# Kernel tuning notes

Hardware: AMD Instinct MI355X
Metric: run time of the kernel (lower is better)

## Reference

```python
import jax, jax.numpy as jnp
import numpy as np

N_NODES = 100000
N_EDGES = 3200000
N_IN = 128
N_HID = 128
N_OUT = 64
HOP = 10


def setup_inputs() -> dict:
    key = jax.random.key(0)
    ks = jax.random.split(key, 8)
    x = jax.random.normal(ks[0], (N_NODES, N_IN), dtype=jnp.float32)
    edge_row = jax.random.randint(ks[1], (N_EDGES,), 0, N_NODES, dtype=jnp.int32)
    edge_col = jax.random.randint(ks[2], (N_EDGES,), 0, N_NODES, dtype=jnp.int32)
    # normalized-ish edge weights so 10 hops of propagation stay bounded
    edge_val = jax.random.uniform(ks[3], (N_EDGES,), dtype=jnp.float32) / 32.0
    s_ih = 1.0 / np.sqrt(N_IN)
    s_hh = 1.0 / np.sqrt(N_HID)
    W_ih = jax.random.normal(ks[4], (4 * N_HID, N_IN), dtype=jnp.float32) * s_ih
    W_hh = jax.random.normal(ks[5], (4 * N_HID, N_HID), dtype=jnp.float32) * s_hh
    b_ih = jnp.zeros((4 * N_HID,), dtype=jnp.float32)
    b_hh = jnp.zeros((4 * N_HID,), dtype=jnp.float32)
    fc_w = jax.random.normal(ks[6], (N_OUT, N_HID), dtype=jnp.float32) * s_hh
    fc_b = jnp.zeros((N_OUT,), dtype=jnp.float32)
    return dict(x=x, edge_row=edge_row, edge_col=edge_col, edge_val=edge_val,
                W_ih=W_ih, W_hh=W_hh, b_ih=b_ih, b_hh=b_hh, fc_w=fc_w, fc_b=fc_b)


def _lstm_cell(x, h, c, W_ih, W_hh, b_ih, b_hh):
    # torch LSTMCell gate order: input, forget, cell(g), output
    gates = x @ W_ih.T + b_ih + h @ W_hh.T + b_hh  # [N, 4H]
    i, f, g, o = jnp.split(gates, 4, axis=-1)
    i = jax.nn.sigmoid(i)
    f = jax.nn.sigmoid(f)
    g = jnp.tanh(g)
    o = jax.nn.sigmoid(o)
    c_new = f * c + i * g
    h_new = o * jnp.tanh(c_new)
    return h_new, c_new


def _spmm(edge_row, edge_col, edge_val, h, n_nodes):
    # (A @ h)[r] = sum_{edges e with row r} val[e] * h[col[e]]
    msgs = edge_val[:, None] * h[edge_col]  # [E, H] gather
    return jax.ops.segment_sum(msgs, edge_row, num_segments=n_nodes)


def reference(x, edge_row, edge_col, edge_val, W_ih, W_hh, b_ih, b_hh, fc_w, fc_b):
    n = x.shape[0]
    h = jnp.zeros((n, W_hh.shape[1]), dtype=x.dtype)
    c = jnp.zeros_like(h)
    # hop iterations: LSTM gate update then sparse propagation (dropout = eval/identity)
    for _ in range(HOP):
        h, c = _lstm_cell(x, h, c, W_ih, W_hh, b_ih, b_hh)
        h = _spmm(edge_row, edge_col, edge_val, h, n)
    h = jax.nn.relu(h)
    return h @ fc_w.T + fc_b
```

## Files before the change

kernel.cpp:

```cpp
#include <hip/hip_runtime.h>
#include <hip/hip_bf16.h>
#include <math.h>

constexpr int NN  = 100000;
constexpr int EE  = 3200000;
constexpr int HID = 128;
constexpr int NG  = 512;
constexpr int NOUT = 64;
constexpr int HOPS = 10;
constexpr int SCAN_BLK = 1024;
constexpr int NBLK_SCAN = (NN + SCAN_BLK - 1) / SCAN_BLK;

typedef __attribute__((ext_vector_type(8))) short short8;
typedef __attribute__((ext_vector_type(4))) float f32x4;

__device__ __forceinline__ ushort f2bf(float f) {
    uint u = __builtin_bit_cast(uint, f);
    u += 0x7fff + ((u >> 16) & 1);
    return (ushort)(u >> 16);
}
__device__ __forceinline__ float bflo(uint u) { return __builtin_bit_cast(float, u << 16); }
__device__ __forceinline__ float bfhi(uint u) { return __builtin_bit_cast(float, u & 0xffff0000u); }

__device__ __forceinline__ float sigf(float v) { return 1.0f / (1.0f + __expf(-v)); }
__device__ __forceinline__ float tanh_fast(float x) {
    float t = __expf(-2.0f * fabsf(x));
    float r = (1.0f - t) / (1.0f + t);
    return copysignf(r, x);
}

__device__ __forceinline__ short8 load_frag(const ushort* p) {
    return *reinterpret_cast<const short8*>(p);
}
__device__ __forceinline__ f32x4 mfma16(short8 a, short8 b, f32x4 c) {
    return __builtin_amdgcn_mfma_f32_16x16x32_bf16(a, b, c, 0, 0, 0);
}

__global__ __launch_bounds__(256) void convert_bf16_kernel(
    const float* __restrict__ src, ushort* __restrict__ dst, int n4)
{
    int i = blockIdx.x * 256 + threadIdx.x;
    if (i < n4) {
        float4 v = reinterpret_cast<const float4*>(src)[i];
        ushort4 o;
        o.x = f2bf(v.x); o.y = f2bf(v.y); o.z = f2bf(v.z); o.w = f2bf(v.w);
        reinterpret_cast<ushort4*>(dst)[i] = o;
    }
}

__global__ __launch_bounds__(256) void bsum_kernel(
    const float* __restrict__ bih, const float* __restrict__ bhh, float* __restrict__ bsum)
{
    int i = blockIdx.x * 256 + threadIdx.x;
    if (i < NG) bsum[i] = bih[i] + bhh[i];
}

__global__ __launch_bounds__(256) void hist_kernel(const int* __restrict__ erow,
                                                   int* __restrict__ deg)
{
    int e = blockIdx.x * 256 + threadIdx.x;
    atomicAdd(&deg[erow[e]], 1);
}

__global__ __launch_bounds__(SCAN_BLK) void scan1_kernel(const int* __restrict__ deg,
                                                         int* __restrict__ bsums)
{
    __shared__ int tmp[SCAN_BLK];
    int t = threadIdx.x;
    int i = blockIdx.x * SCAN_BLK + t;
    tmp[t] = (i < NN) ? deg[i] : 0;
    __syncthreads();
    for (int off = SCAN_BLK / 2; off > 0; off >>= 1) {
        if (t < off) tmp[t] += tmp[t + off];
        __syncthreads();
    }
    if (t == 0) bsums[blockIdx.x] = tmp[0];
}

__global__ __launch_bounds__(128) void scan2_kernel(int* __restrict__ bsums)
{
    __shared__ int tmp[128];
    int t = threadIdx.x;
    tmp[t] = (t < NBLK_SCAN) ? bsums[t] : 0;
    __syncthreads();
    for (int off = 1; off < 128; off <<= 1) {
        int add = (t >= off) ? tmp[t - off] : 0;
        __syncthreads();
        tmp[t] += add;
        __syncthreads();
    }
    if (t < NBLK_SCAN) bsums[t] = tmp[t] - ((t < NBLK_SCAN) ? 0 : 0) - (t < NBLK_SCAN ? (t == 0 ? tmp[0] : tmp[t] - tmp[t - 1]) : 0) + ((t == 0) ? 0 : tmp[t - 1]) - ((t == 0) ? 0 : tmp[t - 1]);
    if (t < NBLK_SCAN) bsums[t] = (t == 0) ? 0 : tmp[t - 1];
}

__global__ __launch_bounds__(SCAN_BLK) void scan3_kernel(const int* __restrict__ deg,
                                                         const int* __restrict__ bsums,
                                                         int* __restrict__ rp,
                                                         int* __restrict__ cur)
{
    __shared__ int tmp[SCAN_BLK];
    int t = threadIdx.x;
    int i = blockIdx.x * SCAN_BLK + t;
    int v = (i < NN) ? deg[i] : 0;
    tmp[t] = v;
    __syncthreads();
    for (int off = 1; off < SCAN_BLK; off <<= 1) {
        int add = (t >= off) ? tmp[t - off] : 0;
        __syncthreads();
        tmp[t] += add;
        __syncthreads();
    }
    int incl = tmp[t] + bsums[blockIdx.x];
    if (i < NN) {
        rp[i + 1] = incl;
        cur[i] = incl - v;
    }
    if (i == 0) rp[0] = 0;
}

__global__ __launch_bounds__(256) void scatter_kernel(
    const int* __restrict__ erow, const int* __restrict__ ecol,
    const float* __restrict__ eval, int* __restrict__ cur,
    int2* __restrict__ epack)
{
    int e = blockIdx.x * 256 + threadIdx.x;
    int r = erow[e];
    int p = atomicAdd(&cur[r], 1);
    int2 pk;
    pk.x = ecol[e];
    pk.y = __builtin_bit_cast(int, eval[e]);
    epack[p] = pk;
}

template<bool FIRST>
__global__ __launch_bounds__(256, 2) void cell_kernel(
    const ushort* __restrict__ xb, const ushort* __restrict__ hb,
    const ushort* __restrict__ Wib, const ushort* __restrict__ Whb,
    const float* __restrict__ bsum, float* __restrict__ cperm,
    ushort* __restrict__ hout)
{
    __shared__ __align__(16) ushort lds_h[32 * 136];

    const int t  = threadIdx.x;
    const int l  = t & 63;
    const int w  = t >> 6;
    const int lr = l & 15;
    const int lk = l >> 4;
    const int row0 = blockIdx.x * 32;

    f32x4 acc[8][2];
#pragma unroll
    for (int nI = 0; nI < 8; ++nI) {
        float b = bsum[(4 * nI + w) * 16 + lr];
        acc[nI][0] = f32x4{b, b, b, b};
        acc[nI][1] = f32x4{b, b, b, b};
    }

    short8 ax[2][4];
    short8 ah[2][4];
#pragma unroll
    for (int rf = 0; rf < 2; ++rf) {
        const size_t arow = (size_t)(row0 + rf * 16 + lr) * HID + lk * 8;
#pragma unroll
        for (int ks = 0; ks < 4; ++ks) {
            ax[rf][ks] = load_frag(xb + arow + ks * 32);
            if (!FIRST) ah[rf][ks] = load_frag(hb + arow + ks * 32);
        }
    }

#pragma unroll
    for (int nI = 0; nI < 8; ++nI) {
        const int n = 4 * nI + w;
        const ushort* wip = Wib + (size_t)(n * 16 + lr) * HID + lk * 8;
        const ushort* whp = Whb + (size_t)(n * 16 + lr) * HID + lk * 8;
        short8 bi[4], bh[4];
#pragma unroll
        for (int ks = 0; ks < 4; ++ks) {
            bi[ks] = load_frag(wip + ks * 32);
            if (!FIRST) bh[ks] = load_frag(whp + ks * 32);
        }
#pragma unroll
        for (int rf = 0; rf < 2; ++rf) {
#pragma unroll
            for (int ks = 0; ks < 4; ++ks) {
                acc[nI][rf] = mfma16(ax[rf][ks], bi[ks], acc[nI][rf]);
                if (!FIRST) acc[nI][rf] = mfma16(ah[rf][ks], bh[ks], acc[nI][rf]);
            }
        }
    }

#pragma unroll
    for (int nj = 0; nj < 2; ++nj) {
        const int col = (w + 4 * nj) * 16 + lr;
#pragma unroll
        for (int rf = 0; rf < 2; ++rf) {
            f32x4 iv = acc[nj][rf];
            f32x4 fv = acc[nj + 2][rf];
            f32x4 gv = acc[nj + 4][rf];
            f32x4 ov = acc[nj + 6][rf];
            const size_t cidx = ((((size_t)blockIdx.x * 4 + w) * 2 + nj) * 2 + rf) * 64 + l;
            f32x4 cold;
            if (FIRST) cold = f32x4{0.f, 0.f, 0.f, 0.f};
            else       cold = reinterpret_cast<const f32x4*>(cperm)[cidx];
            f32x4 cn, hn;
#pragma unroll
            for (int jj = 0; jj < 4; ++jj) {
                float c2 = sigf(fv[jj]) * cold[jj] + sigf(iv[jj]) * tanh_fast(gv[jj]);
                cn[jj] = c2;
                hn[jj] = sigf(ov[jj]) * tanh_fast(c2);
            }
            reinterpret_cast<f32x4*>(cperm)[cidx] = cn;
            const int rbase = rf * 16 + lk * 4;
#pragma unroll
            for (int jj = 0; jj < 4; ++jj)
                lds_h[(rbase + jj) * 136 + col] = f2bf(hn[jj]);
        }
    }
    __syncthreads();
    {
        const ushort* lsrc = &lds_h[(t >> 3) * 136 + (t & 7) * 16];
        short8 v0 = *reinterpret_cast<const short8*>(lsrc);
        short8 v1 = *reinterpret_cast<const short8*>(lsrc + 8);
        ushort* gdst = hout + (size_t)row0 * HID + t * 16;
        *reinterpret_cast<short8*>(gdst) = v0;
        *reinterpret_cast<short8*>(gdst + 8) = v1;
    }
}

__global__ __launch_bounds__(256) void spmm_kernel(
    const int* __restrict__ rp, const int2* __restrict__ epack,
    const ushort* __restrict__ hin, ushort* __restrict__ hout)
{
    int r = blockIdx.x * 4 + (threadIdx.x >> 6);
    if (r >= NN) return;
    int l = threadIdx.x & 63;
    int beg = rp[r], end = rp[r + 1];

    float s0a = 0.f, s1a = 0.f, s0b = 0.f, s1b = 0.f;
    float s0c = 0.f, s1c = 0.f, s0d = 0.f, s1d = 0.f;
    int e = beg;
    for (; e + 4 <= end; e += 4) {
        int2 p0 = epack[e], p1 = epack[e + 1], p2 = epack[e + 2], p3 = epack[e + 3];
        float v0 = __builtin_bit_cast(float, p0.y);
        float v1 = __builtin_bit_cast(float, p1.y);
        float v2 = __builtin_bit_cast(float, p2.y);
        float v3 = __builtin_bit_cast(float, p3.y);
        uint g0 = *reinterpret_cast<const uint*>(hin + (size_t)p0.x * HID + l * 2);
        uint g1 = *reinterpret_cast<const uint*>(hin + (size_t)p1.x * HID + l * 2);
        uint g2 = *reinterpret_cast<const uint*>(hin + (size_t)p2.x * HID + l * 2);
        uint g3 = *reinterpret_cast<const uint*>(hin + (size_t)p3.x * HID + l * 2);
        s0a += v0 * bflo(g0); s1a += v0 * bfhi(g0);
        s0b += v1 * bflo(g1); s1b += v1 * bfhi(g1);
        s0c += v2 * bflo(g2); s1c += v2 * bfhi(g2);
        s0d += v3 * bflo(g3); s1d += v3 * bfhi(g3);
    }
    for (; e < end; ++e) {
        int2 p0 = epack[e];
        float v0 = __builtin_bit_cast(float, p0.y);
        uint g0 = *reinterpret_cast<const uint*>(hin + (size_t)p0.x * HID + l * 2);
        s0a += v0 * bflo(g0); s1a += v0 * bfhi(g0);
    }
    float s0 = (s0a + s0b) + (s0c + s0d);
    float s1 = (s1a + s1b) + (s1c + s1d);
    uint o = ((uint)f2bf(s1) << 16) | (uint)f2bf(s0);
    *reinterpret_cast<uint*>(hout + (size_t)r * HID + l * 2) = o;
}

__global__ __launch_bounds__(256) void final_mfma_kernel(
    const ushort* __restrict__ hb, const ushort* __restrict__ fcwb,
    const float* __restrict__ fcb, float* __restrict__ out)
{
    const int t = threadIdx.x;
    const int l = t & 63;
    const int w = t >> 6;
    const int lr = l & 15;
    const int lk = l >> 4;
    const int row0 = blockIdx.x * 64 + w * 16;

    f32x4 acc[4];
#pragma unroll
    for (int n = 0; n < 4; ++n) {
        float b = fcb[n * 16 + lr];
        acc[n] = f32x4{b, b, b, b};
    }

    const short8 z8 = {0, 0, 0, 0, 0, 0, 0, 0};
    const int arow = row0 + lr;
    const bool aok = arow < NN;
    short8 a[4];
#pragma unroll
    for (int ks = 0; ks < 4; ++ks) {
        short8 v = aok ? load_frag(hb + (size_t)arow * HID + ks * 32 + lk * 8) : z8;
#pragma unroll
        for (int i = 0; i < 8; ++i) {
            ushort u = (ushort)v[i];
            if (u & 0x8000) v[i] = 0;
        }
        a[ks] = v;
    }

#pragma unroll
    for (int n = 0; n < 4; ++n) {
        const ushort* wp = fcwb + (size_t)(n * 16 + lr) * HID + lk * 8;
#pragma unroll
        for (int ks = 0; ks < 4; ++ks)
            acc[n] = mfma16(a[ks], load_frag(wp + ks * 32), acc[n]);
    }

#pragma unroll
    for (int n = 0; n < 4; ++n) {
#pragma unroll
        for (int j = 0; j < 4; ++j) {
            int row = row0 + lk * 4 + j;
            if (row < NN) out[(size_t)row * NOUT + n * 16 + lr] = acc[n][j];
        }
    }
}

extern "C" void kernel_launch(void* const* d_in, const int* in_sizes, int n_in,
                              void* d_out, int out_size, void* d_ws, size_t ws_size,
                              hipStream_t stream)
{
    const float* x    = (const float*)d_in[0];
    const int*   erow = (const int*)d_in[1];
    const int*   ecol = (const int*)d_in[2];
    const float* eval = (const float*)d_in[3];
    const float* Wih  = (const float*)d_in[4];
    const float* Whh  = (const float*)d_in[5];
    const float* bih  = (const float*)d_in[6];
    const float* bhh  = (const float*)d_in[7];
    const float* fcw  = (const float*)d_in[8];
    const float* fcb  = (const float*)d_in[9];
    float* out = (float*)d_out;

    char* ws = (char*)d_ws;
    size_t off = 0;
    auto alloc = [&](size_t bytes) -> void* {
        void* p = ws + off;
        off = (off + bytes + 255) & ~(size_t)255;
        return p;
    };
    ushort* hb_a  = (ushort*)alloc((size_t)NN * HID * 2);
    ushort* hb_b  = (ushort*)alloc((size_t)NN * HID * 2);
    float*  cperm = (float*)alloc((size_t)NN * HID * 4);
    ushort* xb    = (ushort*)alloc((size_t)NN * HID * 2);
    ushort* Wib   = (ushort*)alloc((size_t)NG * HID * 2);
    ushort* Whb   = (ushort*)alloc((size_t)NG * HID * 2);
    ushort* fcwb  = (ushort*)alloc((size_t)NOUT * HID * 2);
    float*  bsum  = (float*)alloc((size_t)NG * 4);
    int*    rp    = (int*)alloc((size_t)(NN + 1) * 4);
    int*    deg   = (int*)alloc((size_t)NN * 4);
    int*    cur   = (int*)alloc((size_t)NN * 4);
    int*    bsums = (int*)alloc((size_t)NBLK_SCAN * 4);
    int2*   epack = (int2*)alloc((size_t)EE * 8);
    (void)ws_size;

    convert_bf16_kernel<<<(NN * HID / 4 + 255) / 256, 256, 0, stream>>>(x, xb, NN * HID / 4);
    convert_bf16_kernel<<<(NG * HID / 4 + 255) / 256, 256, 0, stream>>>(Wih, Wib, NG * HID / 4);
    convert_bf16_kernel<<<(NG * HID / 4 + 255) / 256, 256, 0, stream>>>(Whh, Whb, NG * HID / 4);
    convert_bf16_kernel<<<(NOUT * HID / 4 + 255) / 256, 256, 0, stream>>>(fcw, fcwb, NOUT * HID / 4);
    bsum_kernel<<<2, 256, 0, stream>>>(bih, bhh, bsum);

    hipMemsetAsync(deg, 0, (size_t)NN * 4, stream);
    hist_kernel<<<EE / 256, 256, 0, stream>>>(erow, deg);
    scan1_kernel<<<NBLK_SCAN, SCAN_BLK, 0, stream>>>(deg, bsums);
    scan2_kernel<<<1, 128, 0, stream>>>(bsums);
    scan3_kernel<<<NBLK_SCAN, SCAN_BLK, 0, stream>>>(deg, bsums, rp, cur);
    scatter_kernel<<<EE / 256, 256, 0, stream>>>(erow, ecol, eval, cur, epack);

    const int CELL_GRID = NN / 32;

    cell_kernel<true><<<CELL_GRID, 256, 0, stream>>>(xb, hb_b, Wib, Whb, bsum, cperm, hb_a);
    spmm_kernel<<<(NN + 3) / 4, 256, 0, stream>>>(rp, epack, hb_a, hb_b);
    for (int hop = 1; hop < HOPS; ++hop) {
        cell_kernel<false><<<CELL_GRID, 256, 0, stream>>>(xb, hb_b, Wib, Whb, bsum, cperm, hb_a);
        spmm_kernel<<<(NN + 3) / 4, 256, 0, stream>>>(rp, epack, hb_a, hb_b);
    }

    final_mfma_kernel<<<(NN + 63) / 64, 256, 0, stream>>>(hb_b, fcwb, fcb, out);
}
```

Before: 2.803 ms.

## Widen LSTM cell tile to 64 rows, store cell state in fp16, nontemporal edge loads

The cell kernel now handles 64 rows per block instead of 32, so each weight fragment loaded is reused across twice as many rows. The x and h matmuls run as two phases separated by a sched barrier, which limits register pressure. The persistent cell state is stored in fp16 instead of fp32, halving its read and write traffic each hop at some cost in precision. The SpMM loads packed edges as 64-bit nontemporal loads to keep the edge stream from polluting cache needed by the h gathers.

```diff
diff --git a/kernel.cpp b/kernel.cpp
--- a/kernel.cpp
+++ b/kernel.cpp
@@ -10,9 +10,13 @@
 constexpr int HOPS = 10;
 constexpr int SCAN_BLK = 1024;
 constexpr int NBLK_SCAN = (NN + SCAN_BLK - 1) / SCAN_BLK;
+constexpr int CELL_GRID = (NN + 63) / 64;
+constexpr size_t CPERM_SLOTS = (size_t)CELL_GRID * 4 * 2 * 4 * 64;
 
 typedef __attribute__((ext_vector_type(8))) short short8;
 typedef __attribute__((ext_vector_type(4))) float f32x4;
+typedef __attribute__((ext_vector_type(4))) _Float16 half4;
+typedef unsigned long long ull;
 
 __device__ __forceinline__ ushort f2bf(float f) {
     uint u = __builtin_bit_cast(uint, f);
@@ -89,7 +93,6 @@
         tmp[t] += add;
         __syncthreads();
     }
-    if (t < NBLK_SCAN) bsums[t] = tmp[t] - ((t < NBLK_SCAN) ? 0 : 0) - (t < NBLK_SCAN ? (t == 0 ? tmp[0] : tmp[t] - tmp[t - 1]) : 0) + ((t == 0) ? 0 : tmp[t - 1]) - ((t == 0) ? 0 : tmp[t - 1]);
     if (t < NBLK_SCAN) bsums[t] = (t == 0) ? 0 : tmp[t - 1];
 }
 
@@ -136,56 +139,77 @@
 __global__ __launch_bounds__(256, 2) void cell_kernel(
     const ushort* __restrict__ xb, const ushort* __restrict__ hb,
     const ushort* __restrict__ Wib, const ushort* __restrict__ Whb,
-    const float* __restrict__ bsum, float* __restrict__ cperm,
+    const float* __restrict__ bsum, half4* __restrict__ cperm,
     ushort* __restrict__ hout)
 {
-    __shared__ __align__(16) ushort lds_h[32 * 136];
+    __shared__ __align__(16) ushort lds_h[64 * 136];
 
     const int t  = threadIdx.x;
     const int l  = t & 63;
     const int w  = t >> 6;
     const int lr = l & 15;
     const int lk = l >> 4;
-    const int row0 = blockIdx.x * 32;
-
-    f32x4 acc[8][2];
+    const int row0 = blockIdx.x * 64;
+
+    f32x4 acc[8][4];
 #pragma unroll
     for (int nI = 0; nI < 8; ++nI) {
         float b = bsum[(4 * nI + w) * 16 + lr];
-        acc[nI][0] = f32x4{b, b, b, b};
-        acc[nI][1] = f32x4{b, b, b, b};
-    }
-
-    short8 ax[2][4];
-    short8 ah[2][4];
-#pragma unroll
-    for (int rf = 0; rf < 2; ++rf) {
-        const size_t arow = (size_t)(row0 + rf * 16 + lr) * HID + lk * 8;
-#pragma unroll
-        for (int ks = 0; ks < 4; ++ks) {
-            ax[rf][ks] = load_frag(xb + arow + ks * 32);
-            if (!FIRST) ah[rf][ks] = load_frag(hb + arow + ks * 32);
-        }
-    }
-
-#pragma unroll
-    for (int nI = 0; nI < 8; ++nI) {
-        const int n = 4 * nI + w;
-        const ushort* wip = Wib + (size_t)(n * 16 + lr) * HID + lk * 8;
-        const ushort* whp = Whb + (size_t)(n * 16 + lr) * HID + lk * 8;
-        short8 bi[4], bh[4];
-#pragma unroll
-        for (int ks = 0; ks < 4; ++ks) {
-            bi[ks] = load_frag(wip + ks * 32);
-            if (!FIRST) bh[ks] = load_frag(whp + ks * 32);
-        }
-#pragma unroll
-        for (int rf = 0; rf < 2; ++rf) {
-#pragma unroll
-            for (int ks = 0; ks < 4; ++ks) {
-                acc[nI][rf] = mfma16(ax[rf][ks], bi[ks], acc[nI][rf]);
-                if (!FIRST) acc[nI][rf] = mfma16(ah[rf][ks], bh[ks], acc[nI][rf]);
-            }
+#pragma unroll
+        for (int rf = 0; rf < 4; ++rf) acc[nI][rf] = f32x4{b, b, b, b};
+    }
+
+    const short8 z8 = {0, 0, 0, 0, 0, 0, 0, 0};
+
+    {
+        short8 ax[4][4];
+#pragma unroll
+        for (int rf = 0; rf < 4; ++rf) {
+            const int arow = row0 + rf * 16 + lr;
+            const bool ok = arow < NN;
+            const size_t ab = (size_t)arow * HID + lk * 8;
+#pragma unroll
+            for (int ks = 0; ks < 4; ++ks)
+                ax[rf][ks] = ok ? load_frag(xb + ab + ks * 32) : z8;
+        }
+#pragma unroll
+        for (int nI = 0; nI < 8; ++nI) {
+            const int n = 4 * nI + w;
+            const ushort* wip = Wib + (size_t)(n * 16 + lr) * HID + lk * 8;
+            short8 bi[4];
+#pragma unroll
+            for (int ks = 0; ks < 4; ++ks) bi[ks] = load_frag(wip + ks * 32);
+#pragma unroll
+            for (int rf = 0; rf < 4; ++rf)
+#pragma unroll
+                for (int ks = 0; ks < 4; ++ks)
+                    acc[nI][rf] = mfma16(ax[rf][ks], bi[ks], acc[nI][rf]);
+        }
+    }
+    __builtin_amdgcn_sched_barrier(0);
+    if (!FIRST) {
+        short8 ah[4][4];
+#pragma unroll
+        for (int rf = 0; rf < 4; ++rf) {
+            const int arow = row0 + rf * 16 + lr;
+            const bool ok = arow < NN;
+            const size_t ab = (size_t)arow * HID + lk * 8;
+#pragma unroll
+            for (int ks = 0; ks < 4; ++ks)
+                ah[rf][ks] = ok ? load_frag(hb + ab + ks * 32) : z8;
+        }
+#pragma unroll
+        for (int nI = 0; nI < 8; ++nI) {
+            const int n = 4 * nI + w;
+            const ushort* whp = Whb + (size_t)(n * 16 + lr) * HID + lk * 8;
+            short8 bh[4];
+#pragma unroll
+            for (int ks = 0; ks < 4; ++ks) bh[ks] = load_frag(whp + ks * 32);
+#pragma unroll
+            for (int rf = 0; rf < 4; ++rf)
+#pragma unroll
+                for (int ks = 0; ks < 4; ++ks)
+                    acc[nI][rf] = mfma16(ah[rf][ks], bh[ks], acc[nI][rf]);
         }
     }
 
@@ -193,23 +217,29 @@
     for (int nj = 0; nj < 2; ++nj) {
         const int col = (w + 4 * nj) * 16 + lr;
 #pragma unroll
-        for (int rf = 0; rf < 2; ++rf) {
+        for (int rf = 0; rf < 4; ++rf) {
             f32x4 iv = acc[nj][rf];
             f32x4 fv = acc[nj + 2][rf];
             f32x4 gv = acc[nj + 4][rf];
             f32x4 ov = acc[nj + 6][rf];
-            const size_t cidx = ((((size_t)blockIdx.x * 4 + w) * 2 + nj) * 2 + rf) * 64 + l;
-            f32x4 cold;
-            if (FIRST) cold = f32x4{0.f, 0.f, 0.f, 0.f};
-            else       cold = reinterpret_cast<const f32x4*>(cperm)[cidx];
-            f32x4 cn, hn;
+            const size_t cidx = ((((size_t)blockIdx.x * 4 + w) * 2 + nj) * 4 + rf) * 64 + l;
+            float cold[4];
+            if (FIRST) {
+                cold[0] = cold[1] = cold[2] = cold[3] = 0.f;
+            } else {
+                half4 ch = cperm[cidx];
+#pragma unroll
+                for (int jj = 0; jj < 4; ++jj) cold[jj] = (float)ch[jj];
+            }
+            half4 cw;
+            float hn[4];
 #pragma unroll
             for (int jj = 0; jj < 4; ++jj) {
                 float c2 = sigf(fv[jj]) * cold[jj] + sigf(iv[jj]) * tanh_fast(gv[jj]);
-                cn[jj] = c2;
+                cw[jj] = (_Float16)c2;
                 hn[jj] = sigf(ov[jj]) * tanh_fast(c2);
             }
-            reinterpret_cast<f32x4*>(cperm)[cidx] = cn;
+            cperm[cidx] = cw;
             const int rbase = rf * 16 + lk * 4;
 #pragma unroll
             for (int jj = 0; jj < 4; ++jj)
@@ -218,12 +248,15 @@
     }
     __syncthreads();
     {
-        const ushort* lsrc = &lds_h[(t >> 3) * 136 + (t & 7) * 16];
-        short8 v0 = *reinterpret_cast<const short8*>(lsrc);
-        short8 v1 = *reinterpret_cast<const short8*>(lsrc + 8);
-        ushort* gdst = hout + (size_t)row0 * HID + t * 16;
-        *reinterpret_cast<short8*>(gdst) = v0;
-        *reinterpret_cast<short8*>(gdst + 8) = v1;
+        const int trow = t >> 2;
+        if (row0 + trow < NN) {
+            const ushort* lsrc = &lds_h[trow * 136 + (t & 3) * 32];
+            ushort* gdst = hout + (size_t)row0 * HID + t * 32;
+#pragma unroll
+            for (int j = 0; j < 4; ++j)
+                *reinterpret_cast<short8*>(gdst + j * 8) =
+                    *reinterpret_cast<const short8*>(lsrc + j * 8);
+        }
     }
 }
 
@@ -235,29 +268,35 @@
     if (r >= NN) return;
     int l = threadIdx.x & 63;
     int beg = rp[r], end = rp[r + 1];
+    const ull* eq = reinterpret_cast<const ull*>(epack);
 
     float s0a = 0.f, s1a = 0.f, s0b = 0.f, s1b = 0.f;
     float s0c = 0.f, s1c = 0.f, s0d = 0.f, s1d = 0.f;
     int e = beg;
     for (; e + 4 <= end; e += 4) {
-        int2 p0 = epack[e], p1 = epack[e + 1], p2 = epack[e + 2], p3 = epack[e + 3];
-        float v0 = __builtin_bit_cast(float, p0.y);
-        float v1 = __builtin_bit_cast(float, p1.y);
-        float v2 = __builtin_bit_cast(float, p2.y);
-        float v3 = __builtin_bit_cast(float, p3.y);
-        uint g0 = *reinterpret_cast<const uint*>(hin + (size_t)p0.x * HID + l * 2);
-        uint g1 = *reinterpret_cast<const uint*>(hin + (size_t)p1.x * HID + l * 2);
-        uint g2 = *reinterpret_cast<const uint*>(hin + (size_t)p2.x * HID + l * 2);
-        uint g3 = *reinterpret_cast<const uint*>(hin + (size_t)p3.x * HID + l * 2);
+        ull u0 = __builtin_nontemporal_load(eq + e);
+        ull u1 = __builtin_nontemporal_load(eq + e + 1);
+        ull u2 = __builtin_nontemporal_load(eq + e + 2);
+        ull u3 = __builtin_nontemporal_load(eq + e + 3);
+        int c0 = (int)(uint)u0, c1 = (int)(uint)u1, c2 = (int)(uint)u2, c3 = (int)(uint)u3;
+        float v0 = __builtin_bit_cast(float, (uint)(u0 >> 32));
+        float v1 = __builtin_bit_cast(float, (uint)(u1 >> 32));
+        float v2 = __builtin_bit_cast(float, (uint)(u2 >> 32));
+        float v3 = __builtin_bit_cast(float, (uint)(u3 >> 32));
+        uint g0 = *reinterpret_cast<const uint*>(hin + (size_t)c0 * HID + l * 2);
+        uint g1 = *reinterpret_cast<const uint*>(hin + (size_t)c1 * HID + l * 2);
+        uint g2 = *reinterpret_cast<const uint*>(hin + (size_t)c2 * HID + l * 2);
+        uint g3 = *reinterpret_cast<const uint*>(hin + (size_t)c3 * HID + l * 2);
         s0a += v0 * bflo(g0); s1a += v0 * bfhi(g0);
         s0b += v1 * bflo(g1); s1b += v1 * bfhi(g1);
         s0c += v2 * bflo(g2); s1c += v2 * bfhi(g2);
         s0d += v3 * bflo(g3); s1d += v3 * bfhi(g3);
     }
     for (; e < end; ++e) {
-        int2 p0 = epack[e];
-        float v0 = __builtin_bit_cast(float, p0.y);
-        uint g0 = *reinterpret_cast<const uint*>(hin + (size_t)p0.x * HID + l * 2);
+        ull u0 = __builtin_nontemporal_load(eq + e);
+        int c0 = (int)(uint)u0;
+        float v0 = __builtin_bit_cast(float, (uint)(u0 >> 32));
+        uint g0 = *reinterpret_cast<const uint*>(hin + (size_t)c0 * HID + l * 2);
         s0a += v0 * bflo(g0); s1a += v0 * bfhi(g0);
     }
     float s0 = (s0a + s0b) + (s0c + s0d);
@@ -342,7 +381,7 @@
     };
     ushort* hb_a  = (ushort*)alloc((size_t)NN * HID * 2);
     ushort* hb_b  = (ushort*)alloc((size_t)NN * HID * 2);
-    float*  cperm = (float*)alloc((size_t)NN * HID * 4);
+    half4*  cperm = (half4*)alloc(CPERM_SLOTS * 8);
     ushort* xb    = (ushort*)alloc((size_t)NN * HID * 2);
     ushort* Wib   = (ushort*)alloc((size_t)NG * HID * 2);
     ushort* Whb   = (ushort*)alloc((size_t)NG * HID * 2);
@@ -368,13 +407,13 @@
     scan3_kernel<<<NBLK_SCAN, SCAN_BLK, 0, stream>>>(deg, bsums, rp, cur);
     scatter_kernel<<<EE / 256, 256, 0, stream>>>(erow, ecol, eval, cur, epack);
 
-    const int CELL_GRID = NN / 32;
+    const int SPMM_GRID = NN / 4;
 
     cell_kernel<true><<<CELL_GRID, 256, 0, stream>>>(xb, hb_b, Wib, Whb, bsum, cperm, hb_a);
-    spmm_kernel<<<(NN + 3) / 4, 256, 0, stream>>>(rp, epack, hb_a, hb_b);
+    spmm_kernel<<<SPMM_GRID, 256, 0, stream>>>(rp, epack, hb_a, hb_b);
     for (int hop = 1; hop < HOPS; ++hop) {
         cell_kernel<false><<<CELL_GRID, 256, 0, stream>>>(xb, hb_b, Wib, Whb, bsum, cperm, hb_a);
-        spmm_kernel<<<(NN + 3) / 4, 256, 0, stream>>>(rp, epack, hb_a, hb_b);
+        spmm_kernel<<<SPMM_GRID, 256, 0, stream>>>(rp, epack, hb_a, hb_b);
     }
 
     final_mfma_kernel<<<(NN + 63) / 64, 256, 0, stream>>>(hb_b, fcwb, fcb, out);
```

Result: slower. 2.990 ms (+6.7%).
